# Kernel tuning notes

Hardware: AMD Instinct MI355X
Metric: run time of the kernel (lower is better)

Reference implementation:

```python
import jax, jax.numpy as jnp
import numpy as np

B, T, F = 2048, 128, 1
H1, H2 = 128, 64


def lstm_relu(x, W, U, b):
    """Keras LSTM with activation=relu, recurrent_activation=sigmoid.
    x: [B, T, Fin]; W: [Fin, 4H]; U: [H, 4H]; b: [4H]. Gate order i,f,g,o.
    Returns full sequence of hidden states [B, T, H]."""
    Bb = x.shape[0]
    H = U.shape[0]

    def step(carry, xt):
        h, c = carry
        z = xt @ W + h @ U + b  # [B, 4H]
        i, f, g, o = jnp.split(z, 4, axis=-1)
        i = jax.nn.sigmoid(i)
        f = jax.nn.sigmoid(f)
        o = jax.nn.sigmoid(o)
        g = jax.nn.relu(g)
        c = f * c + i * g
        h = o * jax.nn.relu(c)
        return (h, c), h

    h0 = jnp.zeros((Bb, H), x.dtype)
    (_, _), hs = jax.lax.scan(step, (h0, h0), jnp.swapaxes(x, 0, 1))
    return jnp.swapaxes(hs, 0, 1)  # [B, T, H]


def setup_inputs() -> dict:
    key = jax.random.key(0)
    ks = jax.random.split(key, 16)
    s = 0.05  # small init so relu LSTM stays numerically stable
    d = {
        "x": jax.random.normal(ks[0], (B, T, F), jnp.float32),
        "W1": jax.random.normal(ks[1], (F, 4 * H1), jnp.float32) * s,
        "U1": jax.random.normal(ks[2], (H1, 4 * H1), jnp.float32) * s,
        "b1": jnp.zeros((4 * H1,), jnp.float32),
        "W2": jax.random.normal(ks[3], (H1, 4 * H2), jnp.float32) * s,
        "U2": jax.random.normal(ks[4], (H2, 4 * H2), jnp.float32) * s,
        "b2": jnp.zeros((4 * H2,), jnp.float32),
        "W3": jax.random.normal(ks[5], (H2, 4 * H2), jnp.float32) * s,
        "U3": jax.random.normal(ks[6], (H2, 4 * H2), jnp.float32) * s,
        "b3": jnp.zeros((4 * H2,), jnp.float32),
        "W4": jax.random.normal(ks[7], (H2, 4 * H1), jnp.float32) * s,
        "U4": jax.random.normal(ks[8], (H1, 4 * H1), jnp.float32) * s,
        "b4": jnp.zeros((4 * H1,), jnp.float32),
        "Wd": jax.random.normal(ks[9], (H1, 1), jnp.float32) * s,
        "bd": jnp.zeros((1,), jnp.float32),
    }
    return d


def reference(x, W1, U1, b1, W2, U2, b2, W3, U3, b3, W4, U4, b4, Wd, bd):
    h = lstm_relu(x, W1, U1, b1)            # [B, T, 128]
    h = lstm_relu(h, W2, U2, b2)[:, -1]     # return_sequences=False -> [B, 64]
    h = jnp.broadcast_to(h[:, None, :], (h.shape[0], T, h.shape[-1]))  # RepeatVector
    h = lstm_relu(h, W3, U3, b3)            # [B, T, 64]
    h = lstm_relu(h, W4, U4, b4)            # [B, T, 128]
    out = h @ Wd + bd                       # TimeDistributed Dense(1) -> [B, T, 1]
    return out
```

## Files before the change

kernel.cpp:

```cpp
#include <hip/hip_runtime.h>


#define TSEQ 128
#define NTH  512
#define BSTR 408

typedef __attribute__((ext_vector_type(8))) short bf16x8;
typedef __attribute__((ext_vector_type(4))) float f32x4;
typedef __attribute__((ext_vector_type(2))) float f32x2;
typedef __attribute__((ext_vector_type(4))) short s16x4;
typedef unsigned short ushort_t;

#define FB_L1 0
#define FB_L2 256
#define FB_L3 448
#define FB_L4 512
#define FB_W3 896
#define WS_FRAGS 960
#define WS_NEEDED (WS_FRAGS * 1024)

__device__ __forceinline__ ushort_t f2bf(float f) {
    union { float f; unsigned u; } a; a.f = f;
    unsigned r = a.u + 0x7FFF + ((a.u >> 16) & 1);
    return (ushort_t)(r >> 16);
}
__device__ __forceinline__ float bf2f(ushort_t h) {
    union { unsigned u; float f; } a; a.u = ((unsigned)h) << 16;
    return a.f;
}
__device__ __forceinline__ float sigm(float z) { return 1.0f / (1.0f + __expf(-z)); }

__device__ __forceinline__ f32x4 MF(bf16x8 a, bf16x8 b, f32x4 c) {
    return __builtin_amdgcn_mfma_f32_16x16x32_bf16(a, b, c, 0, 0, 0);
}

__global__ void pack_weights(const float* __restrict__ U1, const float* __restrict__ W2,
                             const float* __restrict__ U2, const float* __restrict__ U3,
                             const float* __restrict__ W4, const float* __restrict__ U4,
                             const float* __restrict__ W3, ushort_t* __restrict__ out)
{
    const int f = blockIdx.x;
    const int lane = threadIdx.x;
    int fl, KT, ldm, ksplit = 1 << 30, ld2 = 0;
    const float *base, *base2 = nullptr;
    if (f < 256)      { fl = f;       KT = 4; ldm = 512; base = U1; }
    else if (f < 448) { fl = f - 256; KT = 6; ldm = 256; base = W2; ksplit = 128; base2 = U2; ld2 = 256; }
    else if (f < 512) { fl = f - 448; KT = 2; ldm = 256; base = U3; }
    else if (f < 896) { fl = f - 512; KT = 6; ldm = 512; base = W4; ksplit = 64;  base2 = U4; ld2 = 512; }
    else              { fl = f - 896; KT = 2; ldm = 256; base = W3; }
    const int jt = fl / (KT * 2);
    const int rem = fl % (KT * 2);
    const int kt = rem >> 1;
    const int s = rem & 1;
    const int j = jt * 16 + (lane & 15);
    ushort_t* o = out + f * 512 + lane * 8;
    #pragma unroll
    for (int i = 0; i < 8; ++i) {
        const int k = kt * 32 + (lane >> 4) * 8 + i;
        const float w = (k < ksplit) ? base[k * ldm + j] : base2[(k - ksplit) * ld2 + j];
        const ushort_t hi = f2bf(w);
        o[i] = s ? f2bf(w - bf2f(hi)) : hi;
    }
}

__global__ __launch_bounds__(NTH, 2) void lstm_mfma_kernel(
    const float* __restrict__ x,
    const float* __restrict__ W1, const float* __restrict__ b1,
    const float* __restrict__ b2, const float* __restrict__ b3,
    const float* __restrict__ b4,
    const float* __restrict__ Wd, const float* __restrict__ bd,
    const ushort_t* __restrict__ wsp,
    float* __restrict__ out)
{
    __shared__ __align__(16) ushort_t bU[16][BSTR];
    __shared__ __align__(16) float obuf[16][128];
    __shared__ __align__(16) float xls[16][132];
    __shared__ __align__(16) float w1ls[512], b1ls[512], b4ls[512], b2ls[256];

    const int tid  = threadIdx.x;
    const int wid  = tid >> 6;
    const int lane = tid & 63;
    const int quad = lane >> 4;
    const int l15  = lane & 15;
    const int r0   = blockIdx.x * 16;
    const bf16x8* A = (const bf16x8*)wsp;

    {
        unsigned* p = (unsigned*)&bU[0][0];
        for (int i = tid; i < 16 * BSTR / 2; i += NTH) p[i] = 0u;
        const int srow = tid >> 5, scol = (tid & 31) * 4;
        *(f32x4*)&xls[srow][scol] = *(const f32x4*)&x[(r0 + srow) * TSEQ + scol];
        w1ls[tid] = W1[tid];
        b1ls[tid] = b1[tid];
        b4ls[tid] = b4[tid];
        if (tid < 256) b2ls[tid] = b2[tid];
    }

    const int hcb = 16 * wid + quad * 4;
    const float wd0 = Wd[lane], wd1 = Wd[64 + lane], bd0 = bd[0];

    float c1r[4] = {0.f, 0.f, 0.f, 0.f};
    float c4r[4] = {0.f, 0.f, 0.f, 0.f};

    __syncthreads();

    {
        bf16x8 wL1[16];
        #pragma unroll
        for (int q = 0; q < 4; ++q)
            #pragma unroll
            for (int kt = 0; kt < 4; ++kt)
                wL1[q * 4 + kt] = A[(FB_L1 + ((wid + 8 * q) * 4 + kt) * 2) * 64 + lane];
        bf16x8 wL2[24];
        if (wid < 4) {
            #pragma unroll
            for (int g = 0; g < 4; ++g)
                #pragma unroll
                for (int kt = 0; kt < 6; ++kt)
                    wL2[g * 6 + kt] = A[(FB_L2 + ((4 * g + wid) * 6 + kt) * 2) * 64 + lane];
        }
        float c2r[4] = {0.f, 0.f, 0.f, 0.f};

        for (int t = 0; t < TSEQ; ++t) {
            const int rb1 = (t & 1) * 128, wb1 = 128 - rb1;
            const int h2w = 256 + (t & 1) * 64;
            const int h2r = 256 + (((t & 1) ^ 1)) * 64;

            {
                bf16x8 Bh[4];
                #pragma unroll
                for (int kt = 0; kt < 4; ++kt)
                    Bh[kt] = *(const bf16x8*)&bU[l15][rb1 + kt * 32 + quad * 8];
                const float xr = xls[l15][t];
                f32x4 acc[4];
                #pragma unroll
                for (int q = 0; q < 4; ++q) {
                    const int jb = (wid + 8 * q) * 16 + quad * 4;
                    f32x4 a = *(const f32x4*)&b1ls[jb];
                    a += xr * *(const f32x4*)&w1ls[jb];
                    #pragma unroll
                    for (int kt = 0; kt < 4; ++kt)
                        a = MF(wL1[q * 4 + kt], Bh[kt], a);
                    acc[q] = a;
                }
                s16x4 hv;
                #pragma unroll
                for (int g = 0; g < 4; ++g) {
                    const float zi = acc[0][g];
                    const float zf = acc[1][g];
                    const float zg = acc[2][g];
                    const float zo = acc[3][g];
                    const float c = sigm(zf) * c1r[g] + sigm(zi) * fmaxf(zg, 0.f);
                    c1r[g] = c;
                    const float h = sigm(zo) * fmaxf(c, 0.f);
                    hv[g] = (short)f2bf(h);
                }
                *(s16x4*)&bU[l15][wb1 + hcb] = hv;
            }
            __syncthreads();

            if (wid < 4) {
                bf16x8 Bh[6];
                #pragma unroll
                for (int kt = 0; kt < 4; ++kt)
                    Bh[kt] = *(const bf16x8*)&bU[l15][wb1 + kt * 32 + quad * 8];
                Bh[4] = *(const bf16x8*)&bU[l15][h2r + quad * 8];
                Bh[5] = *(const bf16x8*)&bU[l15][h2r + 32 + quad * 8];
                f32x4 acc[4];
                #pragma unroll
                for (int g = 0; g < 4; ++g) {
                    f32x4 a = *(const f32x4*)&b2ls[(4 * g + wid) * 16 + quad * 4];
                    #pragma unroll
                    for (int kt = 0; kt < 6; ++kt)
                        a = MF(wL2[g * 6 + kt], Bh[kt], a);
                    acc[g] = a;
                }
                s16x4 hv;
                #pragma unroll
                for (int e = 0; e < 4; ++e) {
                    const float zi = acc[0][e];
                    const float zf = acc[1][e];
                    const float zg = acc[2][e];
                    const float zo = acc[3][e];
                    const float c = sigm(zf) * c2r[e] + sigm(zi) * fmaxf(zg, 0.f);
                    c2r[e] = c;
                    const float h = sigm(zo) * fmaxf(c, 0.f);
                    hv[e] = (short)f2bf(h);
                }
                *(s16x4*)&bU[l15][h2w + wid * 16 + quad * 4] = hv;
            }
        }
    }
    __syncthreads();

    f32x4 z3r[4];
    if (wid < 4) {
        const bf16x8 Bh0 = *(const bf16x8*)&bU[l15][320 + quad * 8];
        const bf16x8 Bh1 = *(const bf16x8*)&bU[l15][320 + 32 + quad * 8];
        #pragma unroll
        for (int g = 0; g < 4; ++g) {
            const int jt = 4 * g + wid;
            f32x4 a = *(const f32x4*)&b3[jt * 16 + quad * 4];
            a = MF(A[(FB_W3 + (jt * 2 + 0) * 2) * 64 + lane], Bh0, a);
            a = MF(A[(FB_W3 + (jt * 2 + 1) * 2) * 64 + lane], Bh1, a);
            z3r[g] = a;
        }
    }
    __syncthreads();
    {
        unsigned* p = (unsigned*)&bU[0][0];
        for (int i = tid; i < 16 * BSTR / 2; i += NTH) p[i] = 0u;
        c4r[0] = c4r[1] = c4r[2] = c4r[3] = 0.f;
    }
    __syncthreads();

    {
        bf16x8 wL3[8];
        if (wid < 4) {
            #pragma unroll
            for (int g = 0; g < 4; ++g)
                #pragma unroll
                for (int kt = 0; kt < 2; ++kt)
                    wL3[g * 2 + kt] = A[(FB_L3 + ((4 * g + wid) * 2 + kt) * 2) * 64 + lane];
        }
        bf16x8 wL4[24];
        #pragma unroll
        for (int q = 0; q < 4; ++q)
            #pragma unroll
            for (int kt = 0; kt < 6; ++kt)
                wL4[q * 6 + kt] = A[(FB_L4 + ((wid + 8 * q) * 6 + kt) * 2) * 64 + lane];
        float c3r[4] = {0.f, 0.f, 0.f, 0.f};

        for (int t = 0; t < TSEQ; ++t) {
            const int rb3 = (t & 1) * 64, wb3 = 64 - rb3;
            const int rb4 = 128 + (t & 1) * 128;
            const int wb4 = (rb4 == 128) ? 256 : 128;

            if (wid < 4) {
                const bf16x8 Bh0 = *(const bf16x8*)&bU[l15][rb3 + quad * 8];
                const bf16x8 Bh1 = *(const bf16x8*)&bU[l15][rb3 + 32 + quad * 8];
                f32x4 acc[4];
                #pragma unroll
                for (int g = 0; g < 4; ++g) {
                    f32x4 a = z3r[g];
                    a = MF(wL3[g * 2 + 0], Bh0, a);
                    a = MF(wL3[g * 2 + 1], Bh1, a);
                    acc[g] = a;
                }
                s16x4 hv;
                #pragma unroll
                for (int e = 0; e < 4; ++e) {
                    const float zi = acc[0][e];
                    const float zf = acc[1][e];
                    const float zg = acc[2][e];
                    const float zo = acc[3][e];
                    const float c = sigm(zf) * c3r[e] + sigm(zi) * fmaxf(zg, 0.f);
                    c3r[e] = c;
                    const float h = sigm(zo) * fmaxf(c, 0.f);
                    hv[e] = (short)f2bf(h);
                }
                *(s16x4*)&bU[l15][wb3 + wid * 16 + quad * 4] = hv;
            }
            __syncthreads();

            {
                bf16x8 Bh[6];
                #pragma unroll
                for (int kt = 0; kt < 2; ++kt)
                    Bh[kt] = *(const bf16x8*)&bU[l15][wb3 + kt * 32 + quad * 8];
                #pragma unroll
                for (int kt = 2; kt < 6; ++kt)
                    Bh[kt] = *(const bf16x8*)&bU[l15][rb4 + (kt - 2) * 32 + quad * 8];
                f32x4 acc[4];
                #pragma unroll
                for (int q = 0; q < 4; ++q) {
                    f32x4 a = *(const f32x4*)&b4ls[(wid + 8 * q) * 16 + quad * 4];
                    #pragma unroll
                    for (int kt = 0; kt < 6; ++kt)
                        a = MF(wL4[q * 6 + kt], Bh[kt], a);
                    acc[q] = a;
                }
                s16x4 hv;
                #pragma unroll
                for (int g = 0; g < 4; ++g) {
                    const float zi = acc[0][g];
                    const float zf = acc[1][g];
                    const float zg = acc[2][g];
                    const float zo = acc[3][g];
                    const float c = sigm(zf) * c4r[g] + sigm(zi) * fmaxf(zg, 0.f);
                    c4r[g] = c;
                    const float h = sigm(zo) * fmaxf(c, 0.f);
                    hv[g] = (short)f2bf(h);
                }
                *(s16x4*)&bU[l15][wb4 + hcb] = hv;
            }

            if (t > 0) {
                #pragma unroll
                for (int e = 0; e < 2; ++e) {
                    const int r = wid + 8 * e;
                    const float h0 = bf2f(bU[r][rb4 + lane]);
                    const float h1_ = bf2f(bU[r][rb4 + 64 + lane]);
                    float v = h0 * wd0 + h1_ * wd1;
                    v += __shfl_down(v, 32);
                    v += __shfl_down(v, 16);
                    v += __shfl_down(v, 8);
                    v += __shfl_down(v, 4);
                    v += __shfl_down(v, 2);
                    v += __shfl_down(v, 1);
                    if (lane == 0) obuf[r][t - 1] = v + bd0;
                }
            }
        }
    }
    __syncthreads();
    {
        #pragma unroll
        for (int e = 0; e < 2; ++e) {
            const int r = wid + 8 * e;
            const float h0 = bf2f(bU[r][128 + lane]);
            const float h1_ = bf2f(bU[r][128 + 64 + lane]);
            float v = h0 * wd0 + h1_ * wd1;
            v += __shfl_down(v, 32);
            v += __shfl_down(v, 16);
            v += __shfl_down(v, 8);
            v += __shfl_down(v, 4);
            v += __shfl_down(v, 2);
            v += __shfl_down(v, 1);
            if (lane == 0) obuf[r][127] = v + bd0;
        }
    }
    __syncthreads();
    {
        const int frow = tid >> 5;
        const int fcol = (tid & 31) * 4;
        *(f32x4*)&out[(r0 + frow) * TSEQ + fcol] = *(const f32x4*)&obuf[frow][fcol];
    }
}

#define FNT 512
#define FRPB 8
__global__ __launch_bounds__(FNT, 2) void lstm_stack_kernel(
    const float* __restrict__ x,
    const float* __restrict__ W1, const float* __restrict__ U1, const float* __restrict__ b1,
    const float* __restrict__ W2, const float* __restrict__ U2, const float* __restrict__ b2,
    const float* __restrict__ W3, const float* __restrict__ U3, const float* __restrict__ b3,
    const float* __restrict__ W4, const float* __restrict__ U4, const float* __restrict__ b4,
    const float* __restrict__ Wd, const float* __restrict__ bd,
    float* __restrict__ out)
{
    __shared__ float h1s[FRPB][128], c1s[FRPB][128];
    __shared__ float h2s[FRPB][64],  c2s[FRPB][64];
    __shared__ float h3s[FRPB][64],  c3s[FRPB][64];
    __shared__ float h4s[FRPB][128], c4s[FRPB][128];
    __shared__ float zbf[FRPB][512];
    __shared__ float z3xf[FRPB][256];
    __shared__ float xs[FRPB];

    const int tid = threadIdx.x;
    const int r0  = blockIdx.x * FRPB;
    const int jg  = tid & 255;
    const int grp = tid >> 8;
    const int rb  = grp * 4;

    {
        float* p1 = &h1s[0][0]; float* p2 = &c1s[0][0];
        float* p3 = &h4s[0][0]; float* p4 = &c4s[0][0];
        for (int i = tid; i < FRPB * 128; i += FNT) { p1[i]=0.f; p2[i]=0.f; p3[i]=0.f; p4[i]=0.f; }
        float* q1 = &h2s[0][0]; float* q2 = &c2s[0][0];
        float* q3 = &h3s[0][0]; float* q4 = &c3s[0][0];
        for (int i = tid; i < FRPB * 64; i += FNT) { q1[i]=0.f; q2[i]=0.f; q3[i]=0.f; q4[i]=0.f; }
    }
    __syncthreads();

    const float w1j = W1[tid];
    const float b1j = b1[tid];
    const float b2j = b2[jg];

    for (int t = 0; t < TSEQ; ++t) {
        if (tid < FRPB) xs[tid] = x[(r0 + tid) * TSEQ + t];
        __syncthreads();
        {
            float acc[FRPB];
            #pragma unroll
            for (int r = 0; r < FRPB; ++r) acc[r] = 0.f;
            const float* Uc = U1 + tid;
            #pragma unroll 4
            for (int k4 = 0; k4 < 32; ++k4) {
                const float u0 = Uc[(k4*4+0)*512];
                const float u1 = Uc[(k4*4+1)*512];
                const float u2 = Uc[(k4*4+2)*512];
                const float u3 = Uc[(k4*4+3)*512];
                #pragma unroll
                for (int r = 0; r < FRPB; ++r) {
                    const float4 h = ((const float4*)h1s[r])[k4];
                    acc[r] += h.x*u0 + h.y*u1 + h.z*u2 + h.w*u3;
                }
            }
            #pragma unroll
            for (int r = 0; r < FRPB; ++r) zbf[r][tid] = acc[r] + xs[r]*w1j + b1j;
        }
        __syncthreads();
        for (int e = tid; e < FRPB * 128; e += FNT) {
            const int r = e >> 7, hc = e & 127;
            const float zi = zbf[r][hc], zf = zbf[r][128+hc], zg = zbf[r][256+hc], zo = zbf[r][384+hc];
            const float c = sigm(zf)*c1s[r][hc] + sigm(zi)*fmaxf(zg, 0.f);
            c1s[r][hc] = c;
            h1s[r][hc] = sigm(zo)*fmaxf(c, 0.f);
        }
        __syncthreads();
        {
            float acc[4] = {0.f, 0.f, 0.f, 0.f};
            const float* Wc = W2 + jg;
            #pragma unroll 4
            for (int k4 = 0; k4 < 32; ++k4) {
                const float u0 = Wc[(k4*4+0)*256];
                const float u1 = Wc[(k4*4+1)*256];
                const float u2 = Wc[(k4*4+2)*256];
                const float u3 = Wc[(k4*4+3)*256];
                #pragma unroll
                for (int q = 0; q < 4; ++q) {
                    const float4 h = ((const float4*)h1s[rb+q])[k4];
                    acc[q] += h.x*u0 + h.y*u1 + h.z*u2 + h.w*u3;
                }
            }
            const float* Uc = U2 + jg;
            #pragma unroll 4
            for (int k4 = 0; k4 < 16; ++k4) {
                const float u0 = Uc[(k4*4+0)*256];
                const float u1 = Uc[(k4*4+1)*256];
                const float u2 = Uc[(k4*4+2)*256];
                const float u3 = Uc[(k4*4+3)*256];
                #pragma unroll
                for (int q = 0; q < 4; ++q) {
                    const float4 h = ((const float4*)h2s[rb+q])[k4];
                    acc[q] += h.x*u0 + h.y*u1 + h.z*u2 + h.w*u3;
                }
            }
            #pragma unroll
            for (int q = 0; q < 4; ++q) zbf[rb+q][jg] = acc[q] + b2j;
        }
        __syncthreads();
        {
            const int r = tid >> 6, hc = tid & 63;
            const float zi = zbf[r][hc], zf = zbf[r][64+hc], zg = zbf[r][128+hc], zo = zbf[r][192+hc];
            const float c = sigm(zf)*c2s[r][hc] + sigm(zi)*fmaxf(zg, 0.f);
            c2s[r][hc] = c;
            h2s[r][hc] = sigm(zo)*fmaxf(c, 0.f);
        }
        __syncthreads();
    }
    {
        float acc[4] = {0.f, 0.f, 0.f, 0.f};
        const float* Wc = W3 + jg;
        #pragma unroll 4
        for (int k4 = 0; k4 < 16; ++k4) {
            const float u0 = Wc[(k4*4+0)*256];
            const float u1 = Wc[(k4*4+1)*256];
            const float u2 = Wc[(k4*4+2)*256];
            const float u3 = Wc[(k4*4+3)*256];
            #pragma unroll
            for (int q = 0; q < 4; ++q) {
                const float4 h = ((const float4*)h2s[rb+q])[k4];
                acc[q] += h.x*u0 + h.y*u1 + h.z*u2 + h.w*u3;
            }
        }
        const float b3j = b3[jg];
        #pragma unroll
        for (int q = 0; q < 4; ++q) z3xf[rb+q][jg] = acc[q] + b3j;
    }
    __syncthreads();

    const float b4j = b4[tid];
    const float wd0 = Wd[tid & 63];
    const float wd1 = Wd[64 + (tid & 63)];
    const float bd0 = bd[0];

    for (int t = 0; t < TSEQ; ++t) {
        {
            float acc[4];
            #pragma unroll
            for (int q = 0; q < 4; ++q) acc[q] = z3xf[rb+q][jg];
            const float* Uc = U3 + jg;
            #pragma unroll 4
            for (int k4 = 0; k4 < 16; ++k4) {
                const float u0 = Uc[(k4*4+0)*256];
                const float u1 = Uc[(k4*4+1)*256];
                const float u2 = Uc[(k4*4+2)*256];
                const float u3 = Uc[(k4*4+3)*256];
                #pragma unroll
                for (int q = 0; q < 4; ++q) {
                    const float4 h = ((const float4*)h3s[rb+q])[k4];
                    acc[q] += h.x*u0 + h.y*u1 + h.z*u2 + h.w*u3;
                }
            }
            #pragma unroll
            for (int q = 0; q < 4; ++q) zbf[rb+q][jg] = acc[q];
        }
        __syncthreads();
        {
            const int r = tid >> 6, hc = tid & 63;
            const float zi = zbf[r][hc], zf = zbf[r][64+hc], zg = zbf[r][128+hc], zo = zbf[r][192+hc];
            const float c = sigm(zf)*c3s[r][hc] + sigm(zi)*fmaxf(zg, 0.f);
            c3s[r][hc] = c;
            h3s[r][hc] = sigm(zo)*fmaxf(c, 0.f);
        }
        __syncthreads();
        {
            float acc[FRPB];
            #pragma unroll
            for (int r = 0; r < FRPB; ++r) acc[r] = 0.f;
            const float* Wc = W4 + tid;
            #pragma unroll 4
            for (int k4 = 0; k4 < 16; ++k4) {
                const float u0 = Wc[(k4*4+0)*512];
                const float u1 = Wc[(k4*4+1)*512];
                const float u2 = Wc[(k4*4+2)*512];
                const float u3 = Wc[(k4*4+3)*512];
                #pragma unroll
                for (int r = 0; r < FRPB; ++r) {
                    const float4 h = ((const float4*)h3s[r])[k4];
                    acc[r] += h.x*u0 + h.y*u1 + h.z*u2 + h.w*u3;
                }
            }
            const float* Uc = U4 + tid;
            #pragma unroll 4
            for (int k4 = 0; k4 < 32; ++k4) {
                const float u0 = Uc[(k4*4+0)*512];
                const float u1 = Uc[(k4*4+1)*512];
                const float u2 = Uc[(k4*4+2)*512];
                const float u3 = Uc[(k4*4+3)*512];
                #pragma unroll
                for (int r = 0; r < FRPB; ++r) {
                    const float4 h = ((const float4*)h4s[r])[k4];
                    acc[r] += h.x*u0 + h.y*u1 + h.z*u2 + h.w*u3;
                }
            }
            #pragma unroll
            for (int r = 0; r < FRPB; ++r) zbf[r][tid] = acc[r] + b4j;
        }
        __syncthreads();
        for (int e = tid; e < FRPB * 128; e += FNT) {
            const int r = e >> 7, hc = e & 127;
            const float zi = zbf[r][hc], zf = zbf[r][128+hc], zg = zbf[r][256+hc], zo = zbf[r][384+hc];
            const float c = sigm(zf)*c4s[r][hc] + sigm(zi)*fmaxf(zg, 0.f);
            c4s[r][hc] = c;
            h4s[r][hc] = sigm(zo)*fmaxf(c, 0.f);
        }
        __syncthreads();
        {
            const int wv = tid >> 6, ln = tid & 63;
            float v = h4s[wv][ln]*wd0 + h4s[wv][64+ln]*wd1;
            v += __shfl_down(v, 32, 64);
            v += __shfl_down(v, 16, 64);
            v += __shfl_down(v,  8, 64);
            v += __shfl_down(v,  4, 64);
            v += __shfl_down(v,  2, 64);
            v += __shfl_down(v,  1, 64);
            if (ln == 0) out[(r0 + wv) * TSEQ + t] = v + bd0;
        }
    }
}

extern "C" void kernel_launch(void* const* d_in, const int* in_sizes, int n_in,
                              void* d_out, int out_size, void* d_ws, size_t ws_size,
                              hipStream_t stream) {
    const float* x  = (const float*)d_in[0];
    const float* W1 = (const float*)d_in[1];
    const float* U1 = (const float*)d_in[2];
    const float* b1 = (const float*)d_in[3];
    const float* W2 = (const float*)d_in[4];
    const float* U2 = (const float*)d_in[5];
    const float* b2 = (const float*)d_in[6];
    const float* W3 = (const float*)d_in[7];
    const float* U3 = (const float*)d_in[8];
    const float* b3 = (const float*)d_in[9];
    const float* W4 = (const float*)d_in[10];
    const float* U4 = (const float*)d_in[11];
    const float* b4 = (const float*)d_in[12];
    const float* Wd = (const float*)d_in[13];
    const float* bd = (const float*)d_in[14];
    float* out = (float*)d_out;

    if (ws_size >= (size_t)WS_NEEDED) {
        ushort_t* wsp = (ushort_t*)d_ws;
        pack_weights<<<dim3(WS_FRAGS), dim3(64), 0, stream>>>(U1, W2, U2, U3, W4, U4, W3, wsp);
        lstm_mfma_kernel<<<dim3(2048 / 16), dim3(NTH), 0, stream>>>(
            x, W1, b1, b2, b3, b4, Wd, bd, wsp, out);
    } else {
        lstm_stack_kernel<<<dim3(2048 / FRPB), dim3(FNT), 0, stream>>>(
            x, W1, U1, b1, W2, U2, b2, W3, U3, b3, W4, U4, b4, Wd, bd, out);
    }
}
```

Before: 533.4 us.

## Stage layer-2/3 weights in LDS, use packed bf16 convert, drop occupancy hint

```diff
diff --git a/kernel.cpp b/kernel.cpp
--- a/kernel.cpp
+++ b/kernel.cpp
@@ -32,6 +32,12 @@
 
 __device__ __forceinline__ f32x4 MF(bf16x8 a, bf16x8 b, f32x4 c) {
     return __builtin_amdgcn_mfma_f32_16x16x32_bf16(a, b, c, 0, 0, 0);
+}
+
+__device__ __forceinline__ unsigned cvtpk(float lo, float hi) {
+    unsigned r;
+    asm("v_cvt_pk_bf16_f32 %0, %1, %2" : "=v"(r) : "v"(lo), "v"(hi));
+    return r;
 }
 
 __global__ void pack_weights(const float* __restrict__ U1, const float* __restrict__ W2,
@@ -63,7 +69,7 @@
     }
 }
 
-__global__ __launch_bounds__(NTH, 2) void lstm_mfma_kernel(
+__global__ __launch_bounds__(NTH, 1) void lstm_mfma_kernel(
     const float* __restrict__ x,
     const float* __restrict__ W1, const float* __restrict__ b1,
     const float* __restrict__ b2, const float* __restrict__ b3,
@@ -76,6 +82,7 @@
     __shared__ __align__(16) float obuf[16][128];
     __shared__ __align__(16) float xls[16][132];
     __shared__ __align__(16) float w1ls[512], b1ls[512], b4ls[512], b2ls[256];
+    __shared__ __align__(16) ushort_t wlds[96 * 512];
 
     const int tid  = threadIdx.x;
     const int wid  = tid >> 6;
@@ -94,6 +101,11 @@
         b1ls[tid] = b1[tid];
         b4ls[tid] = b4[tid];
         if (tid < 256) b2ls[tid] = b2[tid];
+        const ushort_t* src = wsp + FB_L2 * 512;
+        for (int i = tid; i < 96 * 64; i += NTH) {
+            const int f = i >> 6, c = (i & 63) * 8;
+            *(bf16x8*)&wlds[f * 512 + c] = *(const bf16x8*)&src[f * 1024 + c];
+        }
     }
 
     const int hcb = 16 * wid + quad * 4;
@@ -111,14 +123,6 @@
             #pragma unroll
             for (int kt = 0; kt < 4; ++kt)
                 wL1[q * 4 + kt] = A[(FB_L1 + ((wid + 8 * q) * 4 + kt) * 2) * 64 + lane];
-        bf16x8 wL2[24];
-        if (wid < 4) {
-            #pragma unroll
-            for (int g = 0; g < 4; ++g)
-                #pragma unroll
-                for (int kt = 0; kt < 6; ++kt)
-                    wL2[g * 6 + kt] = A[(FB_L2 + ((4 * g + wid) * 6 + kt) * 2) * 64 + lane];
-        }
         float c2r[4] = {0.f, 0.f, 0.f, 0.f};
 
         for (int t = 0; t < TSEQ; ++t) {
@@ -143,7 +147,7 @@
                         a = MF(wL1[q * 4 + kt], Bh[kt], a);
                     acc[q] = a;
                 }
-                s16x4 hv;
+                float hg[4];
                 #pragma unroll
                 for (int g = 0; g < 4; ++g) {
                     const float zi = acc[0][g];
@@ -152,10 +156,12 @@
                     const float zo = acc[3][g];
                     const float c = sigm(zf) * c1r[g] + sigm(zi) * fmaxf(zg, 0.f);
                     c1r[g] = c;
-                    const float h = sigm(zo) * fmaxf(c, 0.f);
-                    hv[g] = (short)f2bf(h);
-                }
-                *(s16x4*)&bU[l15][wb1 + hcb] = hv;
+                    hg[g] = sigm(zo) * fmaxf(c, 0.f);
+                }
+                uint2 hv;
+                hv.x = cvtpk(hg[0], hg[1]);
+                hv.y = cvtpk(hg[2], hg[3]);
+                *(uint2*)&bU[l15][wb1 + hcb] = hv;
             }
             __syncthreads();
 
@@ -171,11 +177,13 @@
                 for (int g = 0; g < 4; ++g) {
                     f32x4 a = *(const f32x4*)&b2ls[(4 * g + wid) * 16 + quad * 4];
                     #pragma unroll
-                    for (int kt = 0; kt < 6; ++kt)
-                        a = MF(wL2[g * 6 + kt], Bh[kt], a);
+                    for (int kt = 0; kt < 6; ++kt) {
+                        const bf16x8 w = *(const bf16x8*)&wlds[((4 * g + wid) * 6 + kt) * 512 + lane * 8];
+                        a = MF(w, Bh[kt], a);
+                    }
                     acc[g] = a;
                 }
-                s16x4 hv;
+                float hg[4];
                 #pragma unroll
                 for (int e = 0; e < 4; ++e) {
                     const float zi = acc[0][e];
@@ -184,10 +192,12 @@
                     const float zo = acc[3][e];
                     const float c = sigm(zf) * c2r[e] + sigm(zi) * fmaxf(zg, 0.f);
                     c2r[e] = c;
-                    const float h = sigm(zo) * fmaxf(c, 0.f);
-                    hv[e] = (short)f2bf(h);
-                }
-                *(s16x4*)&bU[l15][h2w + wid * 16 + quad * 4] = hv;
+                    hg[e] = sigm(zo) * fmaxf(c, 0.f);
+                }
+                uint2 hv;
+                hv.x = cvtpk(hg[0], hg[1]);
+                hv.y = cvtpk(hg[2], hg[3]);
+                *(uint2*)&bU[l15][h2w + wid * 16 + quad * 4] = hv;
             }
         }
     }
@@ -211,18 +221,15 @@
         unsigned* p = (unsigned*)&bU[0][0];
         for (int i = tid; i < 16 * BSTR / 2; i += NTH) p[i] = 0u;
         c4r[0] = c4r[1] = c4r[2] = c4r[3] = 0.f;
-    }
-    __syncthreads();
-
-    {
-        bf16x8 wL3[8];
-        if (wid < 4) {
-            #pragma unroll
-            for (int g = 0; g < 4; ++g)
-                #pragma unroll
-                for (int kt = 0; kt < 2; ++kt)
-                    wL3[g * 2 + kt] = A[(FB_L3 + ((4 * g + wid) * 2 + kt) * 2) * 64 + lane];
-        }
+        const ushort_t* src = wsp + FB_L3 * 512;
+        for (int i = tid; i < 32 * 64; i += NTH) {
+            const int f = i >> 6, c = (i & 63) * 8;
+            *(bf16x8*)&wlds[f * 512 + c] = *(const bf16x8*)&src[f * 1024 + c];
+        }
+    }
+    __syncthreads();
+
+    {
         bf16x8 wL4[24];
         #pragma unroll
         for (int q = 0; q < 4; ++q)
@@ -243,11 +250,13 @@
                 #pragma unroll
                 for (int g = 0; g < 4; ++g) {
                     f32x4 a = z3r[g];
-                    a = MF(wL3[g * 2 + 0], Bh0, a);
-                    a = MF(wL3[g * 2 + 1], Bh1, a);
+                    const bf16x8 w0 = *(const bf16x8*)&wlds[((4 * g + wid) * 2 + 0) * 512 + lane * 8];
+                    const bf16x8 w1 = *(const bf16x8*)&wlds[((4 * g + wid) * 2 + 1) * 512 + lane * 8];
+                    a = MF(w0, Bh0, a);
+                    a = MF(w1, Bh1, a);
                     acc[g] = a;
                 }
-                s16x4 hv;
+                float hg[4];
                 #pragma unroll
                 for (int e = 0; e < 4; ++e) {
                     const float zi = acc[0][e];
@@ -256,10 +265,12 @@
                     const float zo = acc[3][e];
                     const float c = sigm(zf) * c3r[e] + sigm(zi) * fmaxf(zg, 0.f);
                     c3r[e] = c;
-                    const float h = sigm(zo) * fmaxf(c, 0.f);
-                    hv[e] = (short)f2bf(h);
-                }
-                *(s16x4*)&bU[l15][wb3 + wid * 16 + quad * 4] = hv;
+                    hg[e] = sigm(zo) * fmaxf(c, 0.f);
+                }
+                uint2 hv;
+                hv.x = cvtpk(hg[0], hg[1]);
+                hv.y = cvtpk(hg[2], hg[3]);
+                *(uint2*)&bU[l15][wb3 + wid * 16 + quad * 4] = hv;
             }
             __syncthreads();
 
@@ -280,7 +291,7 @@
                         a = MF(wL4[q * 6 + kt], Bh[kt], a);
                     acc[q] = a;
                 }
-                s16x4 hv;
+                float hg[4];
                 #pragma unroll
                 for (int g = 0; g < 4; ++g) {
                     const float zi = acc[0][g];
@@ -289,10 +300,12 @@
                     const float zo = acc[3][g];
                     const float c = sigm(zf) * c4r[g] + sigm(zi) * fmaxf(zg, 0.f);
                     c4r[g] = c;
-                    const float h = sigm(zo) * fmaxf(c, 0.f);
-                    hv[g] = (short)f2bf(h);
-                }
-                *(s16x4*)&bU[l15][wb4 + hcb] = hv;
+                    hg[g] = sigm(zo) * fmaxf(c, 0.f);
+                }
+                uint2 hv;
+                hv.x = cvtpk(hg[0], hg[1]);
+                hv.y = cvtpk(hg[2], hg[3]);
+                *(uint2*)&bU[l15][wb4 + hcb] = hv;
             }
 
             if (t > 0) {
```

New measurement: 538.1 us. About the same (+0.9%).
